# Kernel optimization log

Measured on AMD Instinct MI355X. Metric: run time of the kernel, lower is better.

Reference implementation:

```python
import jax, jax.numpy as jnp
import numpy as np

N_QUBITS = 11
DIM = 2 ** N_QUBITS
N_LAYERS = 6  # the circuit repeats the RY/CZ block 6 times


def _apply_ry(state, wire, theta):
    """Apply RY(theta) on `wire`. state: [N] + [2]*N_QUBITS (real, since RY/CZ are real).
    theta is scalar (shared weight) or [N] (per-sample input angle)."""
    half = theta * 0.5
    c, s = jnp.cos(half), jnp.sin(half)
    if c.ndim == 1:  # per-sample angle -> broadcast over remaining qubit axes
        bshape = (c.shape[0],) + (1,) * (N_QUBITS - 1)
        c = c.reshape(bshape)
        s = s.reshape(bshape)
    st = jnp.moveaxis(state, wire + 1, -1)  # [..., 2]
    s0, s1 = st[..., 0], st[..., 1]
    # RY = [[cos, -sin], [sin, cos]] acting on the qubit amplitude pair
    st = jnp.stack([c * s0 - s * s1, s * s0 + c * s1], axis=-1)
    return jnp.moveaxis(st, -1, wire + 1)


def _apply_cz(state, w1, w2):
    """CZ: flip sign of amplitudes where both qubits are |1>."""
    def bit(w):
        shp = [1] * (N_QUBITS + 1)
        shp[w + 1] = 2
        return jnp.array([0.0, 1.0], state.dtype).reshape(shp)
    sign = 1.0 - 2.0 * bit(w1) * bit(w2)
    return state * sign


def _circuit(angles, weights):
    # angles: [N, N_QUBITS] per-sample RY input angles; weights: [N_QUBITS]
    N = angles.shape[0]
    state = jnp.zeros((N, DIM), angles.dtype).at[:, 0].set(1.0)  # |0...0>
    state = state.reshape((N,) + (2,) * N_QUBITS)
    for i in range(N_QUBITS):
        state = _apply_ry(state, i, angles[:, i])
    for _ in range(N_LAYERS):
        for i in range(N_QUBITS):
            state = _apply_ry(state, i, weights[i])
            state = _apply_cz(state, i, (i + 1) % N_QUBITS)
    probs = state.reshape(N, DIM) ** 2  # real state -> |amp|^2
    # PauliZ expectation per wire; wire 0 is the most-significant bit (PennyLane order)
    bits = (jnp.arange(DIM)[:, None] >> jnp.arange(N_QUBITS - 1, -1, -1)[None, :]) & 1
    z = (1.0 - 2.0 * bits).astype(angles.dtype)  # [DIM, N_QUBITS]
    return probs @ z  # [N, N_QUBITS]


def setup_inputs() -> dict:
    key = jax.random.key(0)
    kx, kw = jax.random.split(key)
    x = jax.random.normal(kx, (8, 256, 16), dtype=jnp.float32)
    weights = jax.random.normal(kw, (N_QUBITS,), dtype=jnp.float32)
    return {"x": x, "weights": weights}


def reference(x, weights):
    B, T, _ = x.shape
    # every (b, t) sample is an independent circuit -> batch them all together
    angles = x[:, :, :N_QUBITS].reshape(B * T, N_QUBITS)
    out = _circuit(angles, weights)  # [B*T, N_QUBITS]
    return out.reshape(B, T, N_QUBITS)
```

## Files before the change

kernel.cpp:

```cpp
#include <hip/hip_runtime.h>

#define NQ 11


template <int CTRL>
__device__ __forceinline__ float dpp_mov(float x) {
    const int xi = __builtin_bit_cast(int, x);
    return __builtin_bit_cast(float,
        __builtin_amdgcn_update_dpp(xi, xi, CTRL, 0xf, 0xf, false));
}
#define DPP_XOR1 0xB1
#define DPP_XOR2 0x4E
#define DPP_XOR3 0x1B
#define DPP_XOR7 0x141
#define DPP_XOR8 0x128

#define RY_REG_F(RB, PSB, C, S)                                              \
    _Pragma("unroll")                                                        \
    for (int g = 0; g < 16; ++g) {                                           \
        const int r0 = ((g >> (RB)) << ((RB) + 1)) | (g & ((1 << (RB)) - 1));\
        const int r1 = r0 | (1 << (RB));                                     \
        const float a_ = v[r0], b_ = v[r1];                                  \
        if (r0 & (PSB)) {                                   \
            v[r0] = (C) * a_ + (S) * b_;                                     \
            v[r1] = (S) * a_ - (C) * b_;                                     \
        } else {                                                             \
            v[r0] = (C) * a_ - (S) * b_;                                     \
            v[r1] = (S) * a_ + (C) * b_;                                     \
        }                                                                    \
    }

#define RY_LANE_G(PGET, CM, SM)                                              \
    _Pragma("unroll")                                                        \
    for (int r = 0; r < 32; ++r) {                                           \
        const float pa_ = PGET(v[r]);                                        \
        v[r] = (CM) * v[r] + (SM) * pa_;                                     \
    }

__global__ __launch_bounds__(256, 2) void qru_kernel(
    const float* __restrict__ x,
    const float* __restrict__ w,
    float* __restrict__ out)
{
    const int lane = threadIdx.x & 63;
    const int n    = blockIdx.x * 4 + (threadIdx.x >> 6);

    const float4 xa = *(const float4*)(x + n * 16);
    const float4 xb = *(const float4*)(x + n * 16 + 4);
    const float4 xc = *(const float4*)(x + n * 16 + 8);
    const float xv[NQ] = {xa.x, xa.y, xa.z, xa.w, xb.x, xb.y, xb.z, xb.w,
                          xc.x, xc.y, xc.z};
    float ci[NQ], si[NQ];
#pragma unroll
    for (int q = 0; q < NQ; ++q) {
        const float h = xv[q] * 0.5f;
        si[q] = __sinf(h); ci[q] = __cosf(h);
    }
    float cw[NQ], sw[NQ];
#pragma unroll
    for (int q = 0; q < NQ; ++q) {
        const float h = w[q] * 0.5f;
        sw[q] = __sinf(h); cw[q] = __cosf(h);
    }

    const float laneF =
        ((lane & 32) ? si[5]  : ci[5])  *
        ((lane & 16) ? si[6]  : ci[6])  *
        ((lane & 8)  ? si[7]  : ci[7])  *
        ((lane & 4)  ? si[8]  : ci[8])  *
        ((lane & 2)  ? si[9]  : ci[9])  *
        ((lane & 1)  ? si[10] : ci[10]);

    float v[32];
#pragma unroll
    for (int r = 0; r < 32; ++r) {
        v[r] = laneF * ((r & 16) ? si[0] : ci[0])
                     * ((r & 8)  ? si[1] : ci[1])
                     * ((r & 4)  ? si[2] : ci[2])
                     * ((r & 2)  ? si[3] : ci[3])
                     * ((r & 1)  ? si[4] : ci[4]);
    }

    const float X0m = (lane & 1) ?  sw[0] : -sw[0];
    const float Y0m = (lane & 1) ? -cw[0] :  cw[0];
    const float SS5 = (lane & 32) ?  sw[5] : -sw[5];
    const float C5m = (lane & 32) ? -cw[5] :  cw[5];
    const float C6m  = ((lane & 48) == 48) ? -cw[6]  : cw[6];
    const float S6m  = (lane & 48) ? sw[6]  : -sw[6];
    const float C7m  = ((lane & 24) == 24) ? -cw[7]  : cw[7];
    const float S7m  = (lane & 24) ? sw[7]  : -sw[7];
    const float C8m  = ((lane & 12) == 12) ? -cw[8]  : cw[8];
    const float S8m  = (lane & 12) ? sw[8]  : -sw[8];
    const float C9m  = ((lane & 6)  == 6)  ? -cw[9]  : cw[9];
    const float S9m  = (lane & 6)  ? sw[9]  : -sw[9];
    const float C10m = ((lane & 3)  == 3)  ? -cw[10] : cw[10];
    const float S10m = (lane & 3)  ? sw[10] : -sw[10];

    auto shfl32 = [](float t) { return __shfl_xor(t, 32); };
    auto shfl16 = [](float t) { return __shfl_xor(t, 16); };
    auto dppx8  = [](float t) { return dpp_mov<DPP_XOR8>(t); };
    auto dppx4  = [](float t) { return dpp_mov<DPP_XOR3>(dpp_mov<DPP_XOR7>(t)); };
    auto dppx2  = [](float t) { return dpp_mov<DPP_XOR2>(t); };
    auto dppx1  = [](float t) { return dpp_mov<DPP_XOR1>(t); };

    auto layer = [&](float X0, float Y0) {
#pragma unroll
        for (int g = 0; g < 16; ++g) {
            const float a_ = v[g], b_ = v[g | 16];
            v[g]      = cw[0] * a_ + X0 * b_;
            v[g | 16] = sw[0] * a_ + Y0 * b_;
        }
        RY_REG_F(3, 16, cw[1], sw[1])
        RY_REG_F(2, 8,  cw[2], sw[2])
        RY_REG_F(1, 4,  cw[3], sw[3])
        RY_REG_F(0, 2,  cw[4], sw[4])

#pragma unroll
        for (int r = 0; r < 32; ++r) {
            const float pa_ = shfl32(v[r]);
            v[r] = (r & 1) ? (C5m  * v[r] + sw[5] * pa_)
                           : (cw[5] * v[r] + SS5  * pa_);
        }
        RY_LANE_G(shfl16, C6m,  S6m)
        RY_LANE_G(dppx8,  C7m,  S7m)
        RY_LANE_G(dppx4,  C8m,  S8m)
        RY_LANE_G(dppx2,  C9m,  S9m)
        RY_LANE_G(dppx1,  C10m, S10m)
    };

    layer(-sw[0], cw[0]);
#pragma unroll 1
    for (int l = 1; l < 6; ++l) layer(X0m, Y0m);

    float p[32];
#pragma unroll
    for (int r = 0; r < 32; ++r) p[r] = v[r] * v[r];

    float tot = 0.f;
#pragma unroll
    for (int r = 0; r < 32; ++r) tot += p[r];

    float S4 = 0.f, S3 = 0.f, S2 = 0.f, S1 = 0.f, S0 = 0.f;
#pragma unroll
    for (int r = 0; r < 32; ++r) {
        if (r & 16) S4 += p[r];
        if (r & 8)  S3 += p[r];
        if (r & 4)  S2 += p[r];
        if (r & 2)  S1 += p[r];
        if (r & 1)  S0 += p[r];
    }

    float q[NQ];
    q[0] = tot - 2.f * S4;
    q[1] = tot - 2.f * S3;
    q[2] = tot - 2.f * S2;
    q[3] = tot - 2.f * S1;
    q[4] = tot - 2.f * S0;
    q[5]  = (lane & 32) ? -tot : tot;
    q[6]  = (lane & 16) ? -tot : tot;
    q[7]  = (lane & 8)  ? -tot : tot;
    q[8]  = (lane & 4)  ? -tot : tot;
    q[9]  = (lane & 2)  ? -tot : tot;
    q[10] = (lane & 1)  ? -tot : tot;

#pragma unroll
    for (int wq = 0; wq < NQ; ++wq) {
        float a = q[wq];
        a += __shfl_xor(a, 32);
        a += __shfl_xor(a, 16);
        a += dpp_mov<DPP_XOR8>(a);
        a += dpp_mov<DPP_XOR3>(dpp_mov<DPP_XOR7>(a));
        a += dpp_mov<DPP_XOR2>(a);
        a += dpp_mov<DPP_XOR1>(a);
        q[wq] = a;
    }

    if (lane == 0) {
#pragma unroll
        for (int wq = 0; wq < NQ; ++wq) out[n * 11 + wq] = q[wq];
    }
}

extern "C" void kernel_launch(void* const* d_in, const int* in_sizes, int n_in,
                              void* d_out, int out_size, void* d_ws, size_t ws_size,
                              hipStream_t stream) {
    const float* x = (const float*)d_in[0];
    const float* w = (const float*)d_in[1];
    float* out = (float*)d_out;

    qru_kernel<<<512, 256, 0, stream>>>(x, w, out);
}
```

Before: 28.22 us.

## Pack register amplitudes into float2 pairs to use packed FMA instructions

Repacks the 32 per-lane amplitudes as 16 two-wide float vectors, with qubit 4 held as the intra-pair element. All RY gate updates and the final reductions use packed elementwise FMA on these pairs. The aim is to halve the VALU instruction count by using the packed fp32 math available on CDNA3/4. The cost is extra swizzles: qubit 4 now needs an intra-vector swap, and cross-lane shuffles still move each component separately, which may add moves or raise register pressure.

```diff
diff --git a/kernel.cpp b/kernel.cpp
--- a/kernel.cpp
+++ b/kernel.cpp
@@ -2,6 +2,13 @@
 
 #define NQ 11
 
+
+typedef float f32x2 __attribute__((ext_vector_type(2)));
+
+__device__ __forceinline__ f32x2 b2(float s) { f32x2 r; r.x = s; r.y = s; return r; }
+__device__ __forceinline__ f32x2 fma2(f32x2 a, f32x2 b, f32x2 c) {
+    return __builtin_elementwise_fma(a, b, c);
+}
 
 template <int CTRL>
 __device__ __forceinline__ float dpp_mov(float x) {
@@ -15,26 +22,29 @@
 #define DPP_XOR7 0x141
 #define DPP_XOR8 0x128
 
-#define RY_REG_F(RB, PSB, C, S)                                              \
+#define RY_K_F(KB, KSB, C, S)                                                \
     _Pragma("unroll")                                                        \
-    for (int g = 0; g < 16; ++g) {                                           \
-        const int r0 = ((g >> (RB)) << ((RB) + 1)) | (g & ((1 << (RB)) - 1));\
-        const int r1 = r0 | (1 << (RB));                                     \
-        const float a_ = v[r0], b_ = v[r1];                                  \
-        if (r0 & (PSB)) {                                   \
-            v[r0] = (C) * a_ + (S) * b_;                                     \
-            v[r1] = (S) * a_ - (C) * b_;                                     \
+    for (int g = 0; g < 8; ++g) {                                            \
+        const int k0 = ((g >> (KB)) << ((KB) + 1)) | (g & ((1 << (KB)) - 1));\
+        const int k1 = k0 | (1 << (KB));                                     \
+        const f32x2 a_ = v2[k0], b_ = v2[k1];                                \
+        const f32x2 Cv = b2(C), Sv = b2(S);                                  \
+        if (k0 & (KSB)) {                                   \
+            v2[k0] = fma2(Cv, a_, Sv * b_);                                  \
+            v2[k1] = fma2(Sv, a_, -(Cv * b_));                               \
         } else {                                                             \
-            v[r0] = (C) * a_ - (S) * b_;                                     \
-            v[r1] = (S) * a_ + (C) * b_;                                     \
+            v2[k0] = fma2(Cv, a_, -(Sv * b_));                               \
+            v2[k1] = fma2(Sv, a_, Cv * b_);                                  \
         }                                                                    \
     }
 
-#define RY_LANE_G(PGET, CM, SM)                                              \
+#define RY_LANE2(PGETX, CV, SV)                                              \
     _Pragma("unroll")                                                        \
-    for (int r = 0; r < 32; ++r) {                                           \
-        const float pa_ = PGET(v[r]);                                        \
-        v[r] = (CM) * v[r] + (SM) * pa_;                                     \
+    for (int k = 0; k < 16; ++k) {                                           \
+        f32x2 pa_;                                                           \
+        pa_.x = PGETX(v2[k].x);                                              \
+        pa_.y = PGETX(v2[k].y);                                              \
+        v2[k] = fma2(CV, v2[k], (SV) * pa_);                                 \
     }
 
 __global__ __launch_bounds__(256, 2) void qru_kernel(
@@ -71,30 +81,38 @@
         ((lane & 2)  ? si[9]  : ci[9])  *
         ((lane & 1)  ? si[10] : ci[10]);
 
-    float v[32];
-#pragma unroll
-    for (int r = 0; r < 32; ++r) {
-        v[r] = laneF * ((r & 16) ? si[0] : ci[0])
-                     * ((r & 8)  ? si[1] : ci[1])
-                     * ((r & 4)  ? si[2] : ci[2])
-                     * ((r & 2)  ? si[3] : ci[3])
-                     * ((r & 1)  ? si[4] : ci[4]);
+    f32x2 v2[16];
+#pragma unroll
+    for (int k = 0; k < 16; ++k) {
+        const float base = laneF * ((k & 8) ? si[0] : ci[0])
+                                 * ((k & 4) ? si[1] : ci[1])
+                                 * ((k & 2) ? si[2] : ci[2])
+                                 * ((k & 1) ? si[3] : ci[3]);
+        v2[k].x = base * ci[4];
+        v2[k].y = base * si[4];
     }
 
     const float X0m = (lane & 1) ?  sw[0] : -sw[0];
     const float Y0m = (lane & 1) ? -cw[0] :  cw[0];
     const float SS5 = (lane & 32) ?  sw[5] : -sw[5];
     const float C5m = (lane & 32) ? -cw[5] :  cw[5];
-    const float C6m  = ((lane & 48) == 48) ? -cw[6]  : cw[6];
-    const float S6m  = (lane & 48) ? sw[6]  : -sw[6];
-    const float C7m  = ((lane & 24) == 24) ? -cw[7]  : cw[7];
-    const float S7m  = (lane & 24) ? sw[7]  : -sw[7];
-    const float C8m  = ((lane & 12) == 12) ? -cw[8]  : cw[8];
-    const float S8m  = (lane & 12) ? sw[8]  : -sw[8];
-    const float C9m  = ((lane & 6)  == 6)  ? -cw[9]  : cw[9];
-    const float S9m  = (lane & 6)  ? sw[9]  : -sw[9];
-    const float C10m = ((lane & 3)  == 3)  ? -cw[10] : cw[10];
-    const float S10m = (lane & 3)  ? sw[10] : -sw[10];
+    f32x2 Cv5; Cv5.x = cw[5]; Cv5.y = C5m;
+    f32x2 Sv5; Sv5.x = SS5;   Sv5.y = sw[5];
+    const f32x2 C6v  = b2(((lane & 48) == 48) ? -cw[6]  : cw[6]);
+    const f32x2 S6v  = b2((lane & 48) ? sw[6]  : -sw[6]);
+    const f32x2 C7v  = b2(((lane & 24) == 24) ? -cw[7]  : cw[7]);
+    const f32x2 S7v  = b2((lane & 24) ? sw[7]  : -sw[7]);
+    const f32x2 C8v  = b2(((lane & 12) == 12) ? -cw[8]  : cw[8]);
+    const f32x2 S8v  = b2((lane & 12) ? sw[8]  : -sw[8]);
+    const f32x2 C9v  = b2(((lane & 6)  == 6)  ? -cw[9]  : cw[9]);
+    const f32x2 S9v  = b2((lane & 6)  ? sw[9]  : -sw[9]);
+    const f32x2 C10v = b2(((lane & 3)  == 3)  ? -cw[10] : cw[10]);
+    const f32x2 S10v = b2((lane & 3)  ? sw[10] : -sw[10]);
+
+    f32x2 C4p; C4p.x = cw[4]; C4p.y =  cw[4];
+    f32x2 S4p; S4p.x = -sw[4]; S4p.y = sw[4];
+    f32x2 C4m; C4m.x = cw[4]; C4m.y = -cw[4];
+    f32x2 S4m; S4m.x = sw[4]; S4m.y =  sw[4];
 
     auto shfl32 = [](float t) { return __shfl_xor(t, 32); };
     auto shfl16 = [](float t) { return __shfl_xor(t, 16); };
@@ -104,58 +122,57 @@
     auto dppx1  = [](float t) { return dpp_mov<DPP_XOR1>(t); };
 
     auto layer = [&](float X0, float Y0) {
-#pragma unroll
-        for (int g = 0; g < 16; ++g) {
-            const float a_ = v[g], b_ = v[g | 16];
-            v[g]      = cw[0] * a_ + X0 * b_;
-            v[g | 16] = sw[0] * a_ + Y0 * b_;
+        {
+            const f32x2 c0 = b2(cw[0]), s0 = b2(sw[0]);
+            const f32x2 x0 = b2(X0),    y0 = b2(Y0);
+#pragma unroll
+            for (int k = 0; k < 8; ++k) {
+                const f32x2 a_ = v2[k], b_ = v2[k | 8];
+                v2[k]     = fma2(c0, a_, x0 * b_);
+                v2[k | 8] = fma2(s0, a_, y0 * b_);
+            }
         }
-        RY_REG_F(3, 16, cw[1], sw[1])
-        RY_REG_F(2, 8,  cw[2], sw[2])
-        RY_REG_F(1, 4,  cw[3], sw[3])
-        RY_REG_F(0, 2,  cw[4], sw[4])
-
-#pragma unroll
-        for (int r = 0; r < 32; ++r) {
-            const float pa_ = shfl32(v[r]);
-            v[r] = (r & 1) ? (C5m  * v[r] + sw[5] * pa_)
-                           : (cw[5] * v[r] + SS5  * pa_);
+        RY_K_F(2, 8, cw[1], sw[1])
+        RY_K_F(1, 4, cw[2], sw[2])
+        RY_K_F(0, 2, cw[3], sw[3])
+
+#pragma unroll
+        for (int k = 0; k < 16; ++k) {
+            const f32x2 s_ = __builtin_shufflevector(v2[k], v2[k], 1, 0);
+            v2[k] = (k & 1) ? fma2(C4m, v2[k], S4m * s_)
+                            : fma2(C4p, v2[k], S4p * s_);
         }
-        RY_LANE_G(shfl16, C6m,  S6m)
-        RY_LANE_G(dppx8,  C7m,  S7m)
-        RY_LANE_G(dppx4,  C8m,  S8m)
-        RY_LANE_G(dppx2,  C9m,  S9m)
-        RY_LANE_G(dppx1,  C10m, S10m)
+
+        RY_LANE2(shfl32, Cv5, Sv5)
+        RY_LANE2(shfl16, C6v, S6v)
+        RY_LANE2(dppx8,  C7v, S7v)
+        RY_LANE2(dppx4,  C8v, S8v)
+        RY_LANE2(dppx2,  C9v, S9v)
+        RY_LANE2(dppx1,  C10v, S10v)
     };
 
     layer(-sw[0], cw[0]);
 #pragma unroll 1
     for (int l = 1; l < 6; ++l) layer(X0m, Y0m);
 
-    float p[32];
-#pragma unroll
-    for (int r = 0; r < 32; ++r) p[r] = v[r] * v[r];
-
-    float tot = 0.f;
-#pragma unroll
-    for (int r = 0; r < 32; ++r) tot += p[r];
-
-    float S4 = 0.f, S3 = 0.f, S2 = 0.f, S1 = 0.f, S0 = 0.f;
-#pragma unroll
-    for (int r = 0; r < 32; ++r) {
-        if (r & 16) S4 += p[r];
-        if (r & 8)  S3 += p[r];
-        if (r & 4)  S2 += p[r];
-        if (r & 2)  S1 += p[r];
-        if (r & 1)  S0 += p[r];
-    }
+    f32x2 T = b2(0.f), A3 = b2(0.f), A2 = b2(0.f), A1 = b2(0.f), A0 = b2(0.f);
+#pragma unroll
+    for (int k = 0; k < 16; ++k) {
+        const f32x2 p = v2[k] * v2[k];
+        T = T + p;
+        if (k & 8) A3 = A3 + p;
+        if (k & 4) A2 = A2 + p;
+        if (k & 2) A1 = A1 + p;
+        if (k & 1) A0 = A0 + p;
+    }
+    const float tot = T.x + T.y;
 
     float q[NQ];
-    q[0] = tot - 2.f * S4;
-    q[1] = tot - 2.f * S3;
-    q[2] = tot - 2.f * S2;
-    q[3] = tot - 2.f * S1;
-    q[4] = tot - 2.f * S0;
+    q[0] = tot - 2.f * (A3.x + A3.y);
+    q[1] = tot - 2.f * (A2.x + A2.y);
+    q[2] = tot - 2.f * (A1.x + A1.y);
+    q[3] = tot - 2.f * (A0.x + A0.y);
+    q[4] = tot - 2.f * T.y;
     q[5]  = (lane & 32) ? -tot : tot;
     q[6]  = (lane & 16) ? -tot : tot;
     q[7]  = (lane & 8)  ? -tot : tot;
```

New measurement: 25.65 us. -9.1%, faster.
